# Kernel optimization log

Hardware: AMD Instinct MI355X
Metric: run time of the kernel (lower is better)

## Reference

```python
import jax, jax.numpy as jnp
import numpy as np

T, B, D, H, O = 512, 256, 1024, 1024, 5


def setup_inputs() -> dict:
    key = jax.random.key(0)
    ks = jax.random.split(key, 7)
    s = 1.0 / np.sqrt(H).astype(np.float32)
    u = lambda k, shape: jax.random.uniform(k, shape, jnp.float32, -s, s)
    return {
        "input": jax.random.normal(ks[0], (T, B, D), jnp.float32),
        "hidden": jnp.zeros((B, H), jnp.float32),
        "state": jnp.zeros((B, H), jnp.float32),
        "W_in": u(ks[1], (H, D)),   # input_scale (Linear(hidden,hidden); D==H)
        "b_in": u(ks[2], (H,)),
        "W_h": u(ks[3], (H, H)),    # hidden_scale
        "b_h": u(ks[4], (H,)),
        "W_o": u(ks[5], (O, H)),    # h2o
        "b_o": u(ks[6], (O,)),
    }


def reference(input, hidden, state, W_in, b_in, W_h, b_h, W_o, b_o):
    # Dropout(0.5) is identity in eval mode.
    # Per timestep: h = sigmoid(hidden_scale(h) + input_scale(x_t))
    def step(h, x_t):
        e = x_t @ W_in.T + b_in              # [B, H]
        h = jax.nn.sigmoid(h @ W_h.T + b_h + e)
        return h, None

    hidden, _ = jax.lax.scan(step, hidden, input)  # scan over T
    out = jax.nn.log_softmax(hidden @ W_o.T + b_o, axis=-1)  # [B, O]
    return (out, hidden, state)
```

## Files before the change

kernel.cpp:

```cpp
#include <hip/hip_runtime.h>

#define T_STEPS 512
#define BATCH   256
#define DIM     1024
#define NOUT    5
#define BH      (BATCH*DIM)

typedef short s16x8 __attribute__((ext_vector_type(8)));
typedef float f32x4 __attribute__((ext_vector_type(4)));
typedef unsigned short u16;
typedef unsigned int   u32;

__device__ __forceinline__ u16 f2bf(float f) {
    union { float f; u32 u; } v; v.f = f;
    u32 r = v.u + 0x7FFFu + ((v.u >> 16) & 1u);
    return (u16)(r >> 16);
}
__device__ __forceinline__ float bf2f(u16 u) {
    union { u32 u; float f; } v; v.u = ((u32)u) << 16;
    return v.f;
}
__device__ __forceinline__ s16x8 cvt8(float4 a, float4 b) {
    s16x8 v;
    v[0]=(short)f2bf(a.x); v[1]=(short)f2bf(a.y); v[2]=(short)f2bf(a.z); v[3]=(short)f2bf(a.w);
    v[4]=(short)f2bf(b.x); v[5]=(short)f2bf(b.y); v[6]=(short)f2bf(b.z); v[7]=(short)f2bf(b.w);
    return v;
}

__device__ __forceinline__ void ldg_cv16_issue(const u16* p, s16x8* dst) {
    asm volatile("global_load_dwordx4 %0, %1, off sc0 sc1"
                 : "=v"(*dst) : "v"(p) : "memory");
}
__device__ __forceinline__ void stg_cv8(u16* p, ushort4 v) {
    asm volatile("global_store_dwordx2 %0, %1, off sc0 sc1"
                 :: "v"(p), "v"(v) : "memory");
}
__device__ __forceinline__ void wait_vm0() {
    asm volatile("s_waitcnt vmcnt(0)" ::: "memory");
}

__global__ __launch_bounds__(256) void cvt_kernel(const float* __restrict__ src,
                                                  u16* __restrict__ dst, int n4) {
    int i = blockIdx.x * 256 + threadIdx.x;
    if (i < n4) {
        float4 x = ((const float4*)src)[i];
        ushort4 o;
        o.x = f2bf(x.x); o.y = f2bf(x.y); o.z = f2bf(x.z); o.w = f2bf(x.w);
        ((ushort4*)dst)[i] = o;
    }
}

#define PADA 88

__global__ __launch_bounds__(256, 2) void gemm_e(
    const float* __restrict__ X,
    const u16*   __restrict__ Wb,
    const float* __restrict__ b_in,
    u16*         __restrict__ E)
{
    __shared__ u16 sA[128 * PADA];
    __shared__ u16 sB[128 * 64];

    const int K = 1024;
    int tid  = threadIdx.x;
    int lane = tid & 63, wv = tid >> 6;
    int lm   = lane & 15, quad = lane >> 4;
    int bm   = blockIdx.x >> 3, bn = blockIdx.x & 7;
    int wm   = wv >> 1, wn = wv & 1;

    float bias[4];
#pragma unroll
    for (int nt = 0; nt < 4; ++nt)
        bias[nt] = b_in[bn*128 + wn*64 + nt*16 + lm];

    f32x4 acc[4][4];
#pragma unroll
    for (int a = 0; a < 4; ++a)
#pragma unroll
        for (int b = 0; b < 4; ++b)
            acc[a][b] = (f32x4){0.f, 0.f, 0.f, 0.f};

    int colB  = (lane & 7) ^ (lane >> 3);
    int rowB0 = lane >> 3;

    for (int kk = 0; kk < K; kk += 64) {
#pragma unroll
        for (int i = 0; i < 4; ++i) {
            int q   = i*4 + wv;
            int row = q*8 + rowB0;
            const u16* gp = Wb + (size_t)(bn*128 + row)*K + kk + colB*8;
            __builtin_amdgcn_global_load_lds(
                (const __attribute__((address_space(1))) void*)gp,
                (__attribute__((address_space(3))) void*)(sB + q*512),
                16, 0, 0);
        }
#pragma unroll
        for (int p = 0; p < 4; ++p) {
            int row = (tid >> 3) + 32*p;
            int k8  = (tid & 7) * 8;
            const float* gp = X + (size_t)(bm*128 + row)*K + kk + k8;
            float4 x0 = ((const float4*)gp)[0];
            float4 x1 = ((const float4*)gp)[1];
            *(s16x8*)&sA[row*PADA + k8] = cvt8(x0, x1);
        }
        __syncthreads();
#pragma unroll
        for (int kc = 0; kc < 2; ++kc) {
            s16x8 af[4], bfr[4];
#pragma unroll
            for (int mt = 0; mt < 4; ++mt) {
                int row = wm*64 + mt*16 + lm;
                af[mt] = *(const s16x8*)&sA[row*PADA + kc*32 + quad*8];
            }
            int c8 = kc*4 + quad;
#pragma unroll
            for (int nt = 0; nt < 4; ++nt) {
                int row = wn*64 + nt*16 + lm;
                bfr[nt] = *(const s16x8*)&sB[row*64 + ((c8 ^ (row & 7)) * 8)];
            }
#pragma unroll
            for (int mt = 0; mt < 4; ++mt)
#pragma unroll
                for (int nt = 0; nt < 4; ++nt)
                    acc[mt][nt] = __builtin_amdgcn_mfma_f32_16x16x32_bf16(
                        af[mt], bfr[nt], acc[mt][nt], 0, 0, 0);
        }
        __syncthreads();
    }
#pragma unroll
    for (int mt = 0; mt < 4; ++mt)
#pragma unroll
        for (int nt = 0; nt < 4; ++nt)
#pragma unroll
            for (int i = 0; i < 4; ++i) {
                int row = bm*128 + wm*64 + mt*16 + quad*4 + i;
                int col = bn*128 + wn*64 + nt*16 + lm;
                E[(size_t)row*1024 + col] = f2bf(acc[mt][nt][i] + bias[nt]);
            }
}

__global__ __launch_bounds__(256, 1) void rnn_phase2(
    const float* __restrict__ h0,
    const float* __restrict__ Wh,
    const float* __restrict__ bh,
    const u16*   __restrict__ E,
    u16*         __restrict__ hbuf,
    u32*         __restrict__ cnt,
    float*       __restrict__ hidden_out)
{
    __shared__ float red[4][16][68];
    int tid  = threadIdx.x;
    int lane = tid & 63, wv = tid >> 6;
    int lm   = lane & 15, quad = lane >> 4;
    int r    = blockIdx.x >> 4, c = blockIdx.x & 15;

    s16x8 wf[4][8];
#pragma unroll
    for (int ct = 0; ct < 4; ++ct)
#pragma unroll
        for (int kc = 0; kc < 8; ++kc) {
            int n = c*64 + ct*16 + lm;
            int k = wv*256 + kc*32 + quad*8;
            const float* p = Wh + (size_t)n*1024 + k;
            float4 x0 = ((const float4*)p)[0];
            float4 x1 = ((const float4*)p)[1];
            wf[ct][kc] = cvt8(x0, x1);
        }

    int m  = tid >> 4;
    int n4 = (tid & 15) * 4;
    float4 bh4 = *(const float4*)&bh[c*64 + n4];
    int rowA = r*16 + lm;
    u32* cptr = cnt + r*32;

    for (int t = 0; t < T_STEPS; ++t) {
        ushort4 e4 = *(const ushort4*)&E[(size_t)t*BH + (size_t)(r*16 + m)*1024 + c*64 + n4];

        if (t > 0) {
            if (tid == 0) {
                u32 target = (u32)(16*t);
                while (__hip_atomic_load(cptr, __ATOMIC_RELAXED, __HIP_MEMORY_SCOPE_AGENT) < target)
                    __builtin_amdgcn_s_sleep(1);
            }
            __syncthreads();
        }

        s16x8 af[8];
        if (t == 0) {
#pragma unroll
            for (int kc = 0; kc < 8; ++kc) {
                const float* p = h0 + (size_t)rowA*1024 + wv*256 + kc*32 + quad*8;
                float4 x0 = ((const float4*)p)[0];
                float4 x1 = ((const float4*)p)[1];
                af[kc] = cvt8(x0, x1);
            }
        } else {
            const u16* hb = hbuf + (size_t)(t & 1)*BH;
#pragma unroll
            for (int kc = 0; kc < 8; ++kc)
                ldg_cv16_issue(&hb[(size_t)rowA*1024 + wv*256 + kc*32 + quad*8], &af[kc]);
            asm volatile("s_waitcnt vmcnt(0)"
                         : "+v"(af[0]), "+v"(af[1]), "+v"(af[2]), "+v"(af[3]),
                           "+v"(af[4]), "+v"(af[5]), "+v"(af[6]), "+v"(af[7])
                         :: "memory");
        }

        f32x4 acc[4];
#pragma unroll
        for (int ct = 0; ct < 4; ++ct) acc[ct] = (f32x4){0.f, 0.f, 0.f, 0.f};
#pragma unroll
        for (int kc = 0; kc < 8; ++kc)
#pragma unroll
            for (int ct = 0; ct < 4; ++ct)
                acc[ct] = __builtin_amdgcn_mfma_f32_16x16x32_bf16(af[kc], wf[ct][kc], acc[ct], 0, 0, 0);

#pragma unroll
        for (int ct = 0; ct < 4; ++ct)
#pragma unroll
            for (int i = 0; i < 4; ++i)
                red[wv][quad*4 + i][ct*16 + lm] = acc[ct][i];
        __syncthreads();

        float4 p0 = *(const float4*)&red[0][m][n4];
        float4 p1 = *(const float4*)&red[1][m][n4];
        float4 p2 = *(const float4*)&red[2][m][n4];
        float4 p3 = *(const float4*)&red[3][m][n4];
        float4 s;
        s.x = p0.x + p1.x + p2.x + p3.x + bh4.x + bf2f(e4.x);
        s.y = p0.y + p1.y + p2.y + p3.y + bh4.y + bf2f(e4.y);
        s.z = p0.z + p1.z + p2.z + p3.z + bh4.z + bf2f(e4.z);
        s.w = p0.w + p1.w + p2.w + p3.w + bh4.w + bf2f(e4.w);
        float4 h;
        h.x = 1.f / (1.f + __expf(-s.x));
        h.y = 1.f / (1.f + __expf(-s.y));
        h.z = 1.f / (1.f + __expf(-s.z));
        h.w = 1.f / (1.f + __expf(-s.w));

        ushort4 hb4;
        hb4.x = f2bf(h.x); hb4.y = f2bf(h.y); hb4.z = f2bf(h.z); hb4.w = f2bf(h.w);
        stg_cv8(&hbuf[(size_t)((t + 1) & 1)*BH + (size_t)(r*16 + m)*1024 + c*64 + n4], hb4);
        if (t == T_STEPS - 1)
            *(float4*)&hidden_out[(size_t)(r*16 + m)*1024 + c*64 + n4] = h;

        wait_vm0();
        __syncthreads();
        if (tid == 0)
            __hip_atomic_fetch_add(cptr, 1u, __ATOMIC_RELAXED, __HIP_MEMORY_SCOPE_AGENT);
    }
}

__global__ __launch_bounds__(64) void head_kernel(const float* __restrict__ h,
                                                  const float* __restrict__ Wo,
                                                  const float* __restrict__ bo,
                                                  float* __restrict__ out)
{
    int b = blockIdx.x, l = threadIdx.x;
    float a0 = 0.f, a1 = 0.f, a2 = 0.f, a3 = 0.f, a4 = 0.f;
    for (int k = l; k < DIM; k += 64) {
        float hv = h[b*DIM + k];
        a0 += hv * Wo[0*DIM + k];
        a1 += hv * Wo[1*DIM + k];
        a2 += hv * Wo[2*DIM + k];
        a3 += hv * Wo[3*DIM + k];
        a4 += hv * Wo[4*DIM + k];
    }
#pragma unroll
    for (int off = 32; off >= 1; off >>= 1) {
        a0 += __shfl_down(a0, off);
        a1 += __shfl_down(a1, off);
        a2 += __shfl_down(a2, off);
        a3 += __shfl_down(a3, off);
        a4 += __shfl_down(a4, off);
    }
    if (l == 0) {
        float v[5] = {a0 + bo[0], a1 + bo[1], a2 + bo[2], a3 + bo[3], a4 + bo[4]};
        float mx = v[0];
#pragma unroll
        for (int o = 1; o < 5; ++o) mx = fmaxf(mx, v[o]);
        float sum = 0.f;
#pragma unroll
        for (int o = 0; o < 5; ++o) sum += __expf(v[o] - mx);
        float lse = mx + __logf(sum);
#pragma unroll
        for (int o = 0; o < 5; ++o) out[b*NOUT + o] = v[o] - lse;
    }
}

extern "C" void kernel_launch(void* const* d_in, const int* in_sizes, int n_in,
                              void* d_out, int out_size, void* d_ws, size_t ws_size,
                              hipStream_t stream)
{
    const float* X   = (const float*)d_in[0];
    const float* h0  = (const float*)d_in[1];
    const float* st  = (const float*)d_in[2];
    const float* Win = (const float*)d_in[3];
    const float* bin = (const float*)d_in[4];
    const float* Wh  = (const float*)d_in[5];
    const float* bhp = (const float*)d_in[6];
    const float* Wo  = (const float*)d_in[7];
    const float* bo  = (const float*)d_in[8];

    char* ws   = (char*)d_ws;
    u32*  cnt  = (u32*)ws;
    u16*  hbuf = (u16*)(ws + 4096);
    u16*  Wbf  = (u16*)(ws + 4096 + (size_t)2*BH*2);
    u16*  E    = (u16*)(ws + 4096 + (size_t)2*BH*2 + (size_t)DIM*DIM*2);

    float* out_lp = (float*)d_out;
    float* out_h  = out_lp + BATCH*NOUT;
    float* out_st = out_h + BH;

    hipMemsetAsync(cnt, 0, 4096, stream);
    cvt_kernel<<<(DIM*DIM/4 + 255)/256, 256, 0, stream>>>(Win, Wbf, DIM*DIM/4);
    gemm_e<<<(T_STEPS*BATCH/128)*8, 256, 0, stream>>>(X, Wbf, bin, E);
    rnn_phase2<<<256, 256, 0, stream>>>(h0, Wh, bhp, E, hbuf, cnt, out_h);
    head_kernel<<<BATCH, 64, 0, stream>>>(out_h, Wo, bo, out_lp);
    hipMemcpyAsync(out_st, st, (size_t)BH*sizeof(float), hipMemcpyDeviceToDevice, stream);
}
```

Before: 2.752 ms.

## Replace shared atomic counter with per-block flags polled wave-parallel

The recurrent kernel now has each block publish its step number to its own cache-line-padded flag with a plain coherent store, instead of incrementing one shared atomic counter per row group. Each wave polls the 16 producer flags in parallel, one per lane, and uses __all, which removes the tid-0 spin plus __syncthreads barrier. The final step skips the bf16 hbuf store and the flag update. The input GEMM also remaps block IDs so that blocks sharing M rows land on the same XCD, aiming for better L2 reuse of X. The cost is more polling traffic, since every wave now reads 16 lines per step.

```diff
diff --git a/kernel.cpp b/kernel.cpp
--- a/kernel.cpp
+++ b/kernel.cpp
@@ -33,6 +33,10 @@
 }
 __device__ __forceinline__ void stg_cv8(u16* p, ushort4 v) {
     asm volatile("global_store_dwordx2 %0, %1, off sc0 sc1"
+                 :: "v"(p), "v"(v) : "memory");
+}
+__device__ __forceinline__ void stg_cv4(u32* p, u32 v) {
+    asm volatile("global_store_dword %0, %1, off sc0 sc1"
                  :: "v"(p), "v"(v) : "memory");
 }
 __device__ __forceinline__ void wait_vm0() {
@@ -65,7 +69,13 @@
     int tid  = threadIdx.x;
     int lane = tid & 63, wv = tid >> 6;
     int lm   = lane & 15, quad = lane >> 4;
-    int bm   = blockIdx.x >> 3, bn = blockIdx.x & 7;
+
+    int bid = blockIdx.x;
+    int xcd = bid & 7;
+    int s   = bid >> 3;
+    int bn  = s & 7;
+    int bm  = (s >> 3) * 8 + xcd;
+
     int wm   = wv >> 1, wn = wv & 1;
 
     float bias[4];
@@ -145,7 +155,7 @@
     const float* __restrict__ bh,
     const u16*   __restrict__ E,
     u16*         __restrict__ hbuf,
-    u32*         __restrict__ cnt,
+    u32*         __restrict__ flags,
     float*       __restrict__ hidden_out)
 {
     __shared__ float red[4][16][68];
@@ -171,18 +181,22 @@
     int n4 = (tid & 15) * 4;
     float4 bh4 = *(const float4*)&bh[c*64 + n4];
     int rowA = r*16 + lm;
-    u32* cptr = cnt + r*32;
+    const u32* fpoll = flags + (size_t)(r*16 + lm)*16;
+    u32*       fown  = flags + (size_t)(r*16 + c)*16;
 
     for (int t = 0; t < T_STEPS; ++t) {
         ushort4 e4 = *(const ushort4*)&E[(size_t)t*BH + (size_t)(r*16 + m)*1024 + c*64 + n4];
 
         if (t > 0) {
-            if (tid == 0) {
-                u32 target = (u32)(16*t);
-                while (__hip_atomic_load(cptr, __ATOMIC_RELAXED, __HIP_MEMORY_SCOPE_AGENT) < target)
-                    __builtin_amdgcn_s_sleep(1);
-            }
-            __syncthreads();
+            u32 target = (u32)t;
+            for (;;) {
+                u32 v;
+                asm volatile("global_load_dword %0, %1, off sc0 sc1"
+                             : "=v"(v) : "v"(fpoll) : "memory");
+                asm volatile("s_waitcnt vmcnt(0)" ::: "memory");
+                if (__all(v >= target)) break;
+                __builtin_amdgcn_s_sleep(1);
+            }
         }
 
         s16x8 af[8];
@@ -236,16 +250,18 @@
         h.z = 1.f / (1.f + __expf(-s.z));
         h.w = 1.f / (1.f + __expf(-s.w));
 
-        ushort4 hb4;
-        hb4.x = f2bf(h.x); hb4.y = f2bf(h.y); hb4.z = f2bf(h.z); hb4.w = f2bf(h.w);
-        stg_cv8(&hbuf[(size_t)((t + 1) & 1)*BH + (size_t)(r*16 + m)*1024 + c*64 + n4], hb4);
-        if (t == T_STEPS - 1)
+        if (t < T_STEPS - 1) {
+            ushort4 hb4;
+            hb4.x = f2bf(h.x); hb4.y = f2bf(h.y); hb4.z = f2bf(h.z); hb4.w = f2bf(h.w);
+            stg_cv8(&hbuf[(size_t)((t + 1) & 1)*BH + (size_t)(r*16 + m)*1024 + c*64 + n4], hb4);
+        } else {
             *(float4*)&hidden_out[(size_t)(r*16 + m)*1024 + c*64 + n4] = h;
+        }
 
         wait_vm0();
         __syncthreads();
-        if (tid == 0)
-            __hip_atomic_fetch_add(cptr, 1u, __ATOMIC_RELAXED, __HIP_MEMORY_SCOPE_AGENT);
+        if (tid == 0 && t < T_STEPS - 1)
+            stg_cv4(fown, (u32)(t + 1));
     }
 }
 
@@ -300,20 +316,20 @@
     const float* Wo  = (const float*)d_in[7];
     const float* bo  = (const float*)d_in[8];
 
-    char* ws   = (char*)d_ws;
-    u32*  cnt  = (u32*)ws;
-    u16*  hbuf = (u16*)(ws + 4096);
-    u16*  Wbf  = (u16*)(ws + 4096 + (size_t)2*BH*2);
-    u16*  E    = (u16*)(ws + 4096 + (size_t)2*BH*2 + (size_t)DIM*DIM*2);
+    char* ws    = (char*)d_ws;
+    u32*  flags = (u32*)ws;
+    u16*  hbuf  = (u16*)(ws + 32768);
+    u16*  Wbf   = (u16*)(ws + 32768 + (size_t)2*BH*2);
+    u16*  E     = (u16*)(ws + 32768 + (size_t)2*BH*2 + (size_t)DIM*DIM*2);
 
     float* out_lp = (float*)d_out;
     float* out_h  = out_lp + BATCH*NOUT;
     float* out_st = out_h + BH;
 
-    hipMemsetAsync(cnt, 0, 4096, stream);
+    hipMemsetAsync(flags, 0, 32768, stream);
     cvt_kernel<<<(DIM*DIM/4 + 255)/256, 256, 0, stream>>>(Win, Wbf, DIM*DIM/4);
     gemm_e<<<(T_STEPS*BATCH/128)*8, 256, 0, stream>>>(X, Wbf, bin, E);
-    rnn_phase2<<<256, 256, 0, stream>>>(h0, Wh, bhp, E, hbuf, cnt, out_h);
+    rnn_phase2<<<256, 256, 0, stream>>>(h0, Wh, bhp, E, hbuf, flags, out_h);
     head_kernel<<<BATCH, 64, 0, stream>>>(out_h, Wo, bo, out_lp);
     hipMemcpyAsync(out_st, st, (size_t)BH*sizeof(float), hipMemcpyDeviceToDevice, stream);
 }
```

After: 2.730 ms. Within noise of the previous version (-0.8%).

## Fuse input GEMM with recurrent loop and replace per-step barrier with data-tagged polling

Applied to the files above, without the earlier changes.

Merges the input-projection GEMM and the recurrence into one persistent launch. The first 256 blocks compute E tiles in timestep order and bump per-timestep counters, while the other 256 blocks run the recurrence and wait only until the E slice they need is ready, so the GEMM overlaps with the serial loop. The per-step global counter barrier is replaced by tagging the sign bits of the bf16 hidden state with a step parity. Consumers spin re-reading hbuf until every tag matches, then mask the tags off, and the reduction LDS buffer is double-buffered. This relies on all 512 blocks being co-resident and on hidden values being non-negative sigmoid outputs; the spin loops can add memory traffic and contend with the GEMM blocks.

```diff
diff --git a/kernel.cpp b/kernel.cpp
--- a/kernel.cpp
+++ b/kernel.cpp
@@ -5,11 +5,16 @@
 #define DIM     1024
 #define NOUT    5
 #define BH      (BATCH*DIM)
+#define TB      (T_STEPS*BATCH)
+#define PADA    88
+#define NWRK    256
 
 typedef short s16x8 __attribute__((ext_vector_type(8)));
 typedef float f32x4 __attribute__((ext_vector_type(4)));
+typedef unsigned int u32;
 typedef unsigned short u16;
-typedef unsigned int   u32;
+typedef u32 u32x4 __attribute__((ext_vector_type(4)));
+typedef u32 u32x2 __attribute__((ext_vector_type(2)));
 
 __device__ __forceinline__ u16 f2bf(float f) {
     union { float f; u32 u; } v; v.f = f;
@@ -27,12 +32,24 @@
     return v;
 }
 
-__device__ __forceinline__ void ldg_cv16_issue(const u16* p, s16x8* dst) {
+__device__ __forceinline__ void ldg_cv16_issue(const u16* p, u32x4* dst) {
     asm volatile("global_load_dwordx4 %0, %1, off sc0 sc1"
                  : "=v"(*dst) : "v"(p) : "memory");
 }
-__device__ __forceinline__ void stg_cv8(u16* p, ushort4 v) {
+__device__ __forceinline__ void ldg_cv8_issue(const u16* p, u32x2* dst) {
+    asm volatile("global_load_dwordx2 %0, %1, off sc0 sc1"
+                 : "=v"(*dst) : "v"(p) : "memory");
+}
+__device__ __forceinline__ void ldg_cv4_issue(const u32* p, u32* dst) {
+    asm volatile("global_load_dword %0, %1, off sc0 sc1"
+                 : "=v"(*dst) : "v"(p) : "memory");
+}
+__device__ __forceinline__ void stg_cv8_u32(u16* p, u32x2 v) {
     asm volatile("global_store_dwordx2 %0, %1, off sc0 sc1"
+                 :: "v"(p), "v"(v) : "memory");
+}
+__device__ __forceinline__ void stg_cv16(u16* p, s16x8 v) {
+    asm volatile("global_store_dwordx4 %0, %1, off sc0 sc1"
                  :: "v"(p), "v"(v) : "memory");
 }
 __device__ __forceinline__ void wait_vm0() {
@@ -50,109 +67,130 @@
     }
 }
 
-#define PADA 88
-
-__global__ __launch_bounds__(256, 2) void gemm_e(
+__global__ __launch_bounds__(256, 2) void rnn_fused(
     const float* __restrict__ X,
     const u16*   __restrict__ Wb,
     const float* __restrict__ b_in,
-    u16*         __restrict__ E)
-{
-    __shared__ u16 sA[128 * PADA];
-    __shared__ u16 sB[128 * 64];
-
-    const int K = 1024;
-    int tid  = threadIdx.x;
-    int lane = tid & 63, wv = tid >> 6;
-    int lm   = lane & 15, quad = lane >> 4;
-    int bm   = blockIdx.x >> 3, bn = blockIdx.x & 7;
-    int wm   = wv >> 1, wn = wv & 1;
-
-    float bias[4];
-#pragma unroll
-    for (int nt = 0; nt < 4; ++nt)
-        bias[nt] = b_in[bn*128 + wn*64 + nt*16 + lm];
-
-    f32x4 acc[4][4];
-#pragma unroll
-    for (int a = 0; a < 4; ++a)
-#pragma unroll
-        for (int b = 0; b < 4; ++b)
-            acc[a][b] = (f32x4){0.f, 0.f, 0.f, 0.f};
-
-    int colB  = (lane & 7) ^ (lane >> 3);
-    int rowB0 = lane >> 3;
-
-    for (int kk = 0; kk < K; kk += 64) {
-#pragma unroll
-        for (int i = 0; i < 4; ++i) {
-            int q   = i*4 + wv;
-            int row = q*8 + rowB0;
-            const u16* gp = Wb + (size_t)(bn*128 + row)*K + kk + colB*8;
-            __builtin_amdgcn_global_load_lds(
-                (const __attribute__((address_space(1))) void*)gp,
-                (__attribute__((address_space(3))) void*)(sB + q*512),
-                16, 0, 0);
-        }
-#pragma unroll
-        for (int p = 0; p < 4; ++p) {
-            int row = (tid >> 3) + 32*p;
-            int k8  = (tid & 7) * 8;
-            const float* gp = X + (size_t)(bm*128 + row)*K + kk + k8;
-            float4 x0 = ((const float4*)gp)[0];
-            float4 x1 = ((const float4*)gp)[1];
-            *(s16x8*)&sA[row*PADA + k8] = cvt8(x0, x1);
-        }
-        __syncthreads();
-#pragma unroll
-        for (int kc = 0; kc < 2; ++kc) {
-            s16x8 af[4], bfr[4];
-#pragma unroll
-            for (int mt = 0; mt < 4; ++mt) {
-                int row = wm*64 + mt*16 + lm;
-                af[mt] = *(const s16x8*)&sA[row*PADA + kc*32 + quad*8];
-            }
-            int c8 = kc*4 + quad;
-#pragma unroll
-            for (int nt = 0; nt < 4; ++nt) {
-                int row = wn*64 + nt*16 + lm;
-                bfr[nt] = *(const s16x8*)&sB[row*64 + ((c8 ^ (row & 7)) * 8)];
-            }
-#pragma unroll
-            for (int mt = 0; mt < 4; ++mt)
-#pragma unroll
-                for (int nt = 0; nt < 4; ++nt)
-                    acc[mt][nt] = __builtin_amdgcn_mfma_f32_16x16x32_bf16(
-                        af[mt], bfr[nt], acc[mt][nt], 0, 0, 0);
-        }
-        __syncthreads();
-    }
-#pragma unroll
-    for (int mt = 0; mt < 4; ++mt)
-#pragma unroll
-        for (int nt = 0; nt < 4; ++nt)
-#pragma unroll
-            for (int i = 0; i < 4; ++i) {
-                int row = bm*128 + wm*64 + mt*16 + quad*4 + i;
-                int col = bn*128 + wn*64 + nt*16 + lm;
-                E[(size_t)row*1024 + col] = f2bf(acc[mt][nt][i] + bias[nt]);
-            }
-}
-
-__global__ __launch_bounds__(256, 1) void rnn_phase2(
+    u16*         __restrict__ E,
     const float* __restrict__ h0,
     const float* __restrict__ Wh,
     const float* __restrict__ bh,
-    const u16*   __restrict__ E,
     u16*         __restrict__ hbuf,
     u32*         __restrict__ cnt,
     float*       __restrict__ hidden_out)
 {
-    __shared__ float red[4][16][68];
+    __shared__ __align__(16) char lds_raw[39936];
+    int bid  = blockIdx.x;
     int tid  = threadIdx.x;
     int lane = tid & 63, wv = tid >> 6;
     int lm   = lane & 15, quad = lane >> 4;
-    int r    = blockIdx.x >> 4, c = blockIdx.x & 15;
+
+    if (bid < NWRK) {
+        u16* sA = (u16*)lds_raw;
+        u16* sB = (u16*)(lds_raw + 128*PADA*2);
+        const int K = 1024;
+        int w   = bid;
+        int xcd = w & 7;
+        int uu  = w >> 3;
+        int vq  = uu & 3;
+        int bn  = uu >> 2;
+        int wm  = wv >> 1, wn = wv & 1;
+        int colB  = (lane & 7) ^ (lane >> 3);
+        int rowB0 = lane >> 3;
+
+        float bias[4];
+#pragma unroll
+        for (int nt = 0; nt < 4; ++nt)
+            bias[nt] = b_in[bn*128 + wn*64 + nt*16 + lm];
+
+        for (int j = 0; j < 32; ++j) {
+            int bm = j*32 + xcd*4 + vq;
+
+            f32x4 acc[4][4];
+#pragma unroll
+            for (int a = 0; a < 4; ++a)
+#pragma unroll
+                for (int b = 0; b < 4; ++b)
+                    acc[a][b] = (f32x4){0.f, 0.f, 0.f, 0.f};
+
+            for (int kk = 0; kk < K; kk += 64) {
+#pragma unroll
+                for (int i = 0; i < 4; ++i) {
+                    int q   = i*4 + wv;
+                    int row = q*8 + rowB0;
+                    const u16* gp = Wb + (size_t)(bn*128 + row)*K + kk + colB*8;
+                    __builtin_amdgcn_global_load_lds(
+                        (const __attribute__((address_space(1))) void*)gp,
+                        (__attribute__((address_space(3))) void*)(sB + q*512),
+                        16, 0, 0);
+                }
+#pragma unroll
+                for (int p = 0; p < 4; ++p) {
+                    int row = (tid >> 3) + 32*p;
+                    int k8  = (tid & 7) * 8;
+                    const float* gp = X + (size_t)(bm*128 + row)*K + kk + k8;
+                    float4 x0 = ((const float4*)gp)[0];
+                    float4 x1 = ((const float4*)gp)[1];
+                    *(s16x8*)&sA[row*PADA + k8] = cvt8(x0, x1);
+                }
+                __syncthreads();
+#pragma unroll
+                for (int kc = 0; kc < 2; ++kc) {
+                    s16x8 af[4], bfr[4];
+#pragma unroll
+                    for (int mt = 0; mt < 4; ++mt) {
+                        int row = wm*64 + mt*16 + lm;
+                        af[mt] = *(const s16x8*)&sA[row*PADA + kc*32 + quad*8];
+                    }
+                    int c8 = kc*4 + quad;
+#pragma unroll
+                    for (int nt = 0; nt < 4; ++nt) {
+                        int row = wn*64 + nt*16 + lm;
+                        bfr[nt] = *(const s16x8*)&sB[row*64 + ((c8 ^ (row & 7)) * 8)];
+                    }
+#pragma unroll
+                    for (int mt = 0; mt < 4; ++mt)
+#pragma unroll
+                        for (int nt = 0; nt < 4; ++nt)
+                            acc[mt][nt] = __builtin_amdgcn_mfma_f32_16x16x32_bf16(
+                                af[mt], bfr[nt], acc[mt][nt], 0, 0, 0);
+                }
+                __syncthreads();
+            }
+
+            u16* csm = (u16*)lds_raw;
+#pragma unroll
+            for (int mt = 0; mt < 4; ++mt)
+#pragma unroll
+                for (int nt = 0; nt < 4; ++nt)
+#pragma unroll
+                    for (int i = 0; i < 4; ++i) {
+                        int row = wm*64 + mt*16 + quad*4 + i;
+                        int col = wn*64 + nt*16 + lm;
+                        csm[row*128 + col] = f2bf(acc[mt][nt][i] + bias[nt]);
+                    }
+            __syncthreads();
+#pragma unroll
+            for (int sIt = 0; sIt < 8; ++sIt) {
+                int flat = sIt*4096 + tid*16;
+                int row  = flat >> 8;
+                int colb = flat & 255;
+                s16x8 vv = *(const s16x8*)(lds_raw + flat);
+                stg_cv16(&E[(size_t)(bm*128 + row)*1024 + bn*128 + colb/2], vv);
+            }
+            wait_vm0();
+            __syncthreads();
+            if (tid == 0)
+                __hip_atomic_fetch_add(cnt + (bm >> 1), 1u,
+                                       __ATOMIC_RELAXED, __HIP_MEMORY_SCOPE_AGENT);
+        }
+        return;
+    }
+
+    typedef float redT[4][16][68];
+    redT* red = (redT*)lds_raw;
+    int rb = bid - NWRK;
+    int r  = rb >> 4, c = rb & 15;
 
     s16x8 wf[4][8];
 #pragma unroll
@@ -167,85 +205,118 @@
             wf[ct][kc] = cvt8(x0, x1);
         }
 
-    int m  = tid >> 4;
-    int n4 = (tid & 15) * 4;
-    float4 bh4 = *(const float4*)&bh[c*64 + n4];
+    int m   = tid >> 4;
+    int n4q = (tid & 15) * 4;
+    float4 bh4 = *(const float4*)&bh[c*64 + n4q];
     int rowA = r*16 + lm;
-    u32* cptr = cnt + r*32;
-
+    size_t aoff = (size_t)rowA*1024 + wv*256 + quad*8;
+    size_t soff = (size_t)(r*16 + m)*1024 + c*64 + n4q;
+
+    if (tid == 0) {
+        for (;;) {
+            u32 a, b;
+            ldg_cv4_issue(cnt + 0, &a);
+            ldg_cv4_issue(cnt + 1, &b);
+            asm volatile("s_waitcnt vmcnt(0)" : "+v"(a), "+v"(b) :: "memory");
+            if (a >= 16u && b >= 16u) break;
+            __builtin_amdgcn_s_sleep(8);
+        }
+    }
+    __syncthreads();
+
+    bool oknext = true;
     for (int t = 0; t < T_STEPS; ++t) {
-        ushort4 e4 = *(const ushort4*)&E[(size_t)t*BH + (size_t)(r*16 + m)*1024 + c*64 + n4];
-
-        if (t > 0) {
-            if (tid == 0) {
-                u32 target = (u32)(16*t);
-                while (__hip_atomic_load(cptr, __ATOMIC_RELAXED, __HIP_MEMORY_SCOPE_AGENT) < target)
-                    __builtin_amdgcn_s_sleep(1);
-            }
-            __syncthreads();
-        }
-
-        s16x8 af[8];
+        u32x2 e4u;
+        u32x4 afu[8];
         if (t == 0) {
+            ldg_cv8_issue(E + soff, &e4u);
 #pragma unroll
             for (int kc = 0; kc < 8; ++kc) {
-                const float* p = h0 + (size_t)rowA*1024 + wv*256 + kc*32 + quad*8;
+                const float* p = h0 + aoff + kc*32;
                 float4 x0 = ((const float4*)p)[0];
                 float4 x1 = ((const float4*)p)[1];
-                af[kc] = cvt8(x0, x1);
+                afu[kc] = __builtin_bit_cast(u32x4, cvt8(x0, x1));
             }
+            asm volatile("s_waitcnt vmcnt(0)" : "+v"(e4u) :: "memory");
         } else {
             const u16* hb = hbuf + (size_t)(t & 1)*BH;
+            const u16* ep = E + (size_t)t*BH + soff;
+            u32 s2 = (u32)t & 3u;
+            u32 expect = ((s2 & 1u) ? 0x8000u : 0u) | ((s2 & 2u) ? 0x80000000u : 0u);
+            bool okc = oknext;
+            bool okn = false;
+            for (;;) {
+#pragma unroll
+                for (int kc = 0; kc < 8; ++kc)
+                    ldg_cv16_issue(hb + aoff + kc*32, &afu[kc]);
+                u32 cN, cC;
+                ldg_cv8_issue(ep, &e4u);
+                ldg_cv4_issue(cnt + t + 1, &cN);
+                ldg_cv4_issue(cnt + t,     &cC);
+                asm volatile("s_waitcnt vmcnt(0)"
+                             : "+v"(afu[0]), "+v"(afu[1]), "+v"(afu[2]), "+v"(afu[3]),
+                               "+v"(afu[4]), "+v"(afu[5]), "+v"(afu[6]), "+v"(afu[7]),
+                               "+v"(e4u), "+v"(cN), "+v"(cC)
+                             :: "memory");
+                bool use = okc;
+                okn = okn | (cN >= 16u);
+                okc = okc | (cC >= 16u);
+                u32x4 bad4 = (u32x4){0u, 0u, 0u, 0u};
+#pragma unroll
+                for (int kc = 0; kc < 8; ++kc)
+                    bad4 |= (afu[kc] ^ expect) & 0x80008000u;
+                u32 bad = bad4[0] | bad4[1] | bad4[2] | bad4[3];
+                if (use && __all(bad == 0u)) break;
+            }
+            oknext = okn;
 #pragma unroll
             for (int kc = 0; kc < 8; ++kc)
-                ldg_cv16_issue(&hb[(size_t)rowA*1024 + wv*256 + kc*32 + quad*8], &af[kc]);
-            asm volatile("s_waitcnt vmcnt(0)"
-                         : "+v"(af[0]), "+v"(af[1]), "+v"(af[2]), "+v"(af[3]),
-                           "+v"(af[4]), "+v"(af[5]), "+v"(af[6]), "+v"(af[7])
-                         :: "memory");
+                afu[kc] &= 0x7FFF7FFFu;
         }
 
         f32x4 acc[4];
 #pragma unroll
         for (int ct = 0; ct < 4; ++ct) acc[ct] = (f32x4){0.f, 0.f, 0.f, 0.f};
 #pragma unroll
-        for (int kc = 0; kc < 8; ++kc)
+        for (int kc = 0; kc < 8; ++kc) {
+            s16x8 a = __builtin_bit_cast(s16x8, afu[kc]);
 #pragma unroll
             for (int ct = 0; ct < 4; ++ct)
-                acc[ct] = __builtin_amdgcn_mfma_f32_16x16x32_bf16(af[kc], wf[ct][kc], acc[ct], 0, 0, 0);
+                acc[ct] = __builtin_amdgcn_mfma_f32_16x16x32_bf16(a, wf[ct][kc], acc[ct], 0, 0, 0);
+        }
 
 #pragma unroll
         for (int ct = 0; ct < 4; ++ct)
 #pragma unroll
             for (int i = 0; i < 4; ++i)
-                red[wv][quad*4 + i][ct*16 + lm] = acc[ct][i];
+                red[t & 1][wv][quad*4 + i][ct*16 + lm] = acc[ct][i];
         __syncthreads();
 
-        float4 p0 = *(const float4*)&red[0][m][n4];
-        float4 p1 = *(const float4*)&red[1][m][n4];
-        float4 p2 = *(const float4*)&red[2][m][n4];
-        float4 p3 = *(const float4*)&red[3][m][n4];
-        float4 s;
-        s.x = p0.x + p1.x + p2.x + p3.x + bh4.x + bf2f(e4.x);
-        s.y = p0.y + p1.y + p2.y + p3.y + bh4.y + bf2f(e4.y);
-        s.z = p0.z + p1.z + p2.z + p3.z + bh4.z + bf2f(e4.z);
-        s.w = p0.w + p1.w + p2.w + p3.w + bh4.w + bf2f(e4.w);
+        float4 p0 = *(const float4*)&red[t & 1][0][m][n4q];
+        float4 p1 = *(const float4*)&red[t & 1][1][m][n4q];
+        float4 p2 = *(const float4*)&red[t & 1][2][m][n4q];
+        float4 p3 = *(const float4*)&red[t & 1][3][m][n4q];
+        float4 sv;
+        sv.x = p0.x + p1.x + p2.x + p3.x + bh4.x + bf2f((u16)(e4u[0] & 0xFFFFu));
+        sv.y = p0.y + p1.y + p2.y + p3.y + bh4.y + bf2f((u16)(e4u[0] >> 16));
+        sv.z = p0.z + p1.z + p2.z + p3.z + bh4.z + bf2f((u16)(e4u[1] & 0xFFFFu));
+        sv.w = p0.w + p1.w + p2.w + p3.w + bh4.w + bf2f((u16)(e4u[1] >> 16));
         float4 h;
-        h.x = 1.f / (1.f + __expf(-s.x));
-        h.y = 1.f / (1.f + __expf(-s.y));
-        h.z = 1.f / (1.f + __expf(-s.z));
-        h.w = 1.f / (1.f + __expf(-s.w));
-
-        ushort4 hb4;
-        hb4.x = f2bf(h.x); hb4.y = f2bf(h.y); hb4.z = f2bf(h.z); hb4.w = f2bf(h.w);
-        stg_cv8(&hbuf[(size_t)((t + 1) & 1)*BH + (size_t)(r*16 + m)*1024 + c*64 + n4], hb4);
-        if (t == T_STEPS - 1)
-            *(float4*)&hidden_out[(size_t)(r*16 + m)*1024 + c*64 + n4] = h;
-
-        wait_vm0();
-        __syncthreads();
-        if (tid == 0)
-            __hip_atomic_fetch_add(cptr, 1u, __ATOMIC_RELAXED, __HIP_MEMORY_SCOPE_AGENT);
+        h.x = 1.f / (1.f + __expf(-sv.x));
+        h.y = 1.f / (1.f + __expf(-sv.y));
+        h.z = 1.f / (1.f + __expf(-sv.z));
+        h.w = 1.f / (1.f + __expf(-sv.w));
+
+        if (t < T_STEPS - 1) {
+            u32 s3   = (u32)(t + 1) & 3u;
+            u32 mask = ((s3 & 1u) ? 0x8000u : 0u) | ((s3 & 2u) ? 0x80000000u : 0u);
+            u32x2 st;
+            st[0] = ((u32)f2bf(h.x) | ((u32)f2bf(h.y) << 16)) | mask;
+            st[1] = ((u32)f2bf(h.z) | ((u32)f2bf(h.w) << 16)) | mask;
+            stg_cv8_u32(&hbuf[(size_t)((t + 1) & 1)*BH + soff], st);
+        } else {
+            *(float4*)&hidden_out[soff] = h;
+        }
     }
 }
 
@@ -300,20 +371,26 @@
     const float* Wo  = (const float*)d_in[7];
     const float* bo  = (const float*)d_in[8];
 
-    char* ws   = (char*)d_ws;
-    u32*  cnt  = (u32*)ws;
-    u16*  hbuf = (u16*)(ws + 4096);
-    u16*  Wbf  = (u16*)(ws + 4096 + (size_t)2*BH*2);
-    u16*  E    = (u16*)(ws + 4096 + (size_t)2*BH*2 + (size_t)DIM*DIM*2);
+    char*  ws     = (char*)d_ws;
+    size_t off_hb = 32768;
+    size_t off_wb = off_hb + (size_t)2*BH*2;
+    size_t off_e  = off_wb + (size_t)DIM*DIM*2;
+
+    u32* cnt  = (u32*)ws;
+    u16* hbuf = (u16*)(ws + off_hb);
+    u16* Wbf  = (u16*)(ws + off_wb);
+    u16* E    = (u16*)(ws + off_e);
 
     float* out_lp = (float*)d_out;
     float* out_h  = out_lp + BATCH*NOUT;
     float* out_st = out_h + BH;
 
-    hipMemsetAsync(cnt, 0, 4096, stream);
+    hipMemsetAsync(ws, 0, 32768, stream);
+    hipMemsetAsync(hbuf, 0, (size_t)2*BH*2, stream);
     cvt_kernel<<<(DIM*DIM/4 + 255)/256, 256, 0, stream>>>(Win, Wbf, DIM*DIM/4);
-    gemm_e<<<(T_STEPS*BATCH/128)*8, 256, 0, stream>>>(X, Wbf, bin, E);
-    rnn_phase2<<<256, 256, 0, stream>>>(h0, Wh, bhp, E, hbuf, cnt, out_h);
+
+    rnn_fused<<<512, 256, 0, stream>>>(X, Wbf, bin, E, h0, Wh, bhp, hbuf, cnt, out_h);
+
     head_kernel<<<BATCH, 64, 0, stream>>>(out_h, Wo, bo, out_lp);
     hipMemcpyAsync(out_st, st, (size_t)BH*sizeof(float), hipMemcpyDeviceToDevice, stream);
 }
```

Measured after the change: 2.607 ms. -5.3%, faster.
